# Kernel optimization log

Measured on AMD Instinct MI355X. Metric: run time of the kernel, lower is better.

Reference implementation:

```python
import jax, jax.numpy as jnp
import numpy as np

BATCH, IN_SIZE, CH, DIM, MODES, LAYERS, PROJ, OUT = 16, 1, 128, 128, 32, 4, 128, 1


def setup_inputs() -> dict:
    key = jax.random.key(0)
    ks = jax.random.split(key, 12)
    scale = 1.0 / (CH * CH)
    inp = {
        "z": jax.random.normal(ks[0], (BATCH, IN_SIZE, DIM, DIM), dtype=jnp.float32),
        # Lifting: pointwise linear input_size -> channels
        "lift_w": jax.random.normal(ks[1], (CH, IN_SIZE), dtype=jnp.float32) / np.sqrt(IN_SIZE),
        "lift_b": jnp.zeros((CH,), dtype=jnp.float32),
        # Spectral conv weights per layer, two mode corners, complex stored as real/imag
        "wr1": scale * jax.random.normal(ks[2], (LAYERS, CH, CH, MODES, MODES), dtype=jnp.float32),
        "wi1": scale * jax.random.normal(ks[3], (LAYERS, CH, CH, MODES, MODES), dtype=jnp.float32),
        "wr2": scale * jax.random.normal(ks[4], (LAYERS, CH, CH, MODES, MODES), dtype=jnp.float32),
        "wi2": scale * jax.random.normal(ks[5], (LAYERS, CH, CH, MODES, MODES), dtype=jnp.float32),
        # Projection: channels -> projection_size -> output_size (pointwise MLP)
        "pw1": jax.random.normal(ks[6], (PROJ, CH), dtype=jnp.float32) / np.sqrt(CH),
        "pb1": jnp.zeros((PROJ,), dtype=jnp.float32),
        "pw2": jax.random.normal(ks[7], (OUT, PROJ), dtype=jnp.float32) / np.sqrt(PROJ),
        "pb2": jnp.zeros((OUT,), dtype=jnp.float32),
    }
    return inp


def _spectral_conv(v, w1, w2, modes, size):
    # v: [b, c, X, Y] real; rfft2 over last two dims (norm='backward')
    vf = jnp.fft.rfft2(v, norm="backward")  # [b, c, X, Y//2+1] complex
    of = jnp.zeros_like(vf)
    # low-frequency corner
    of = of.at[:, :, :modes, :modes].set(
        jnp.einsum("bixy,ioxy->boxy", vf[:, :, :modes, :modes], w1))
    # high (negative) frequency corner along first spatial axis
    of = of.at[:, :, -modes:, :modes].set(
        jnp.einsum("bixy,ioxy->boxy", vf[:, :, -modes:, :modes], w2))
    return jnp.fft.irfft2(of, s=(size, size), norm="backward")


def reference(z, lift_w, lift_b, wr1, wi1, wr2, wi2, pw1, pb1, pw2, pb2):
    n_layers = wr1.shape[0]
    modes = wr1.shape[-1]
    size = z.shape[-1]
    # Lifting: [b, in, x, y] -> [b, ch, x, y]
    v = jnp.einsum("bixy,ci->bcxy", z, lift_w) + lift_b[None, :, None, None]
    out = v
    for l in range(n_layers):
        w1 = wr1[l] + 1j * wi1[l]
        w2 = wr2[l] + 1j * wi2[l]
        out = _spectral_conv(out, w1, w2, modes, size)
    # Projection MLP (pointwise over grid)
    h = jnp.einsum("bcxy,pc->bpxy", out, pw1) + pb1[None, :, None, None]
    h = jax.nn.gelu(h)
    out = jnp.einsum("bpxy,op->boxy", h, pw2) + pb2[None, :, None, None]
    return out
```

## Files before the change

### kernel.cpp

```cpp
#include <hip/hip_runtime.h>
#include <math.h>

#define B 16
#define CH 128
#define DIM 128
#define MODES 32
#define NLAYERS 4
#define PROJ 128
#define U 64
#define KY 32
#define NMODE (U*KY)
#define N2 (DIM*DIM)
#define PG 32
#define PPG (PROJ/PG)

__device__ __forceinline__ void async16(const void* g, void* l) {
  __builtin_amdgcn_global_load_lds((const __attribute__((address_space(1))) unsigned int*)g,
                                   (__attribute__((address_space(3))) unsigned int*)l, 16, 0, 0);
}

__global__ __launch_bounds__(256) void k_zf1(const float* __restrict__ z,
                                             float2* __restrict__ t1) {
  __shared__ float zrow[16][DIM];
  __shared__ float2 tw[DIM];
  int bid = blockIdx.x;
  int b = bid >> 3, xt = bid & 7;
  int x0 = xt * 16;
  int t = threadIdx.x;
  if (t < 128) {
    float ang = (float)(2.0 * M_PI) * (float)t / 128.0f;
    tw[t] = make_float2(cosf(ang), sinf(ang));
  }
  for (int e = t; e < 16 * DIM / 4; e += 256)
    ((float4*)&zrow[0][0])[e] = ((const float4*)&z[b * N2 + x0 * DIM])[e];
  __syncthreads();
  #pragma unroll
  for (int j = 0; j < 2; ++j) {
    int it = t + j * 256;
    int x_l = it >> 5, ky = it & 31;
    float tr = 0.f, ti = 0.f;
    for (int y = 0; y < DIM; ++y) {
      float v = zrow[x_l][y];
      float2 w = tw[(ky * y) & 127];
      tr += v * w.x;
      ti -= v * w.y;
    }
    t1[((size_t)b * DIM + x0 + x_l) * KY + ky] = make_float2(tr, ti);
  }
}

__global__ __launch_bounds__(256) void k_zf2(const float2* __restrict__ t1,
                                             float* __restrict__ zfr, float* __restrict__ zfi) {
  __shared__ float2 t1s[DIM][KY];
  __shared__ float2 tw[DIM];
  int bid = blockIdx.x;
  int b = bid >> 1, uh = bid & 1;
  int t = threadIdx.x;
  if (t < 128) {
    float ang = (float)(2.0 * M_PI) * (float)t / 128.0f;
    tw[t] = make_float2(cosf(ang), sinf(ang));
  }
  for (int e = t; e < DIM * KY / 2; e += 256)
    ((float4*)&t1s[0][0])[e] = ((const float4*)&t1[(size_t)b * DIM * KY])[e];
  __syncthreads();
  #pragma unroll
  for (int j = 0; j < 4; ++j) {
    int m = t + j * 256;
    int u_l = m >> 5, ky = m & 31;
    int u = uh * 32 + u_l;
    int kx = (u < 32) ? u : (u + 64);
    float ar = 0.f, ai = 0.f;
    for (int x = 0; x < DIM; ++x) {
      float2 v = t1s[x][ky];
      float2 w = tw[(kx * x) & 127];
      ar += v.x * w.x + v.y * w.y;
      ai += v.y * w.x - v.x * w.y;
    }
    zfr[b * NMODE + u * KY + ky] = ar;
    zfi[b * NMODE + u * KY + ky] = ai;
  }
}

__global__ __launch_bounds__(256) void k_lift(const float* __restrict__ zfr, const float* __restrict__ zfi,
                                              const float* __restrict__ lw, const float* __restrict__ lb,
                                              float2* __restrict__ vcout) {
  int idx = blockIdx.x * 256 + threadIdx.x;
  if (idx >= B * CH * NMODE) return;
  int m = idx & (NMODE - 1);
  int c = (idx >> 11) & 127;
  int b = idx >> 18;
  float w = lw[c];
  float re = w * zfr[b * NMODE + m];
  float im = w * zfi[b * NMODE + m];
  if (m == 0) re += 16384.f * lb[c];
  vcout[idx] = make_float2(re, im);
}

__global__ __launch_bounds__(256) void k_spec(const float2* __restrict__ vc,
                                              const float* __restrict__ wr1, const float* __restrict__ wi1,
                                              const float* __restrict__ wr2, const float* __restrict__ wi2,
                                              float2* __restrict__ oc) {
  __shared__ float4 ring4[4][1024];
  int bid = blockIdx.x;
  int u = ((bid & 7) << 3) | ((bid >> 3) & 7);
  int ot = bid >> 6;
  int o0 = ot * 16;
  int kxw = u & 31;
  const float* wr = (u >= 32) ? wr2 : wr1;
  const float* wi = (u >= 32) ? wi2 : wi1;
  int t = threadIdx.x;
  int ky = t & 31, bh = (t >> 5) & 1, wv = t >> 6;
  int lane = t & 63;
  float accR[4][8] = {}, accI[4][8] = {};

  #define STAGE(c)                                                                   \
    if ((c) < 64) {                                                                  \
      int bf_ = (c) & 3;                                                             \
      int i0_ = (c) * 2;                                                             \
      char* dst0 = (char*)&ring4[0][0] + (size_t)bf_ * 16384;                        \
      _Pragma("unroll")                                                              \
      for (int n = 0; n < 4; ++n) {                                                  \
        int nu = wv * 4 + n;                                                         \
        if (nu < 8) {                                                                \
          int row = nu * 8 + (lane >> 3);                           \
          int ri = row >> 5, il = (row >> 4) & 1, o_l = row & 15;                    \
          int ky4 = (lane & 7) * 4;                                                  \
          const float* src = (ri ? wi : wr) +                                        \
            (((size_t)(i0_ + il) * CH + o0 + o_l) * MODES + kxw) * MODES + ky4;      \
          async16(src, dst0 + (size_t)nu * 1024 + lane * 16);                        \
        } else {                                                                     \
          int nv = nu - 8;                                                           \
          int row = nv * 4 + (lane >> 4);                               \
          int il = row >> 4, bl = row & 15;                                          \
          int ky2 = (lane & 15) * 2;                                                 \
          const float2* src = vc + ((size_t)bl * CH + i0_ + il) * NMODE +            \
                              u * KY + ky2;                                          \
          async16(src, dst0 + 8192 + (size_t)nv * 1024 + lane * 16);                 \
        }                                                                            \
      }                                                                              \
    }

  #define COMPUTE(bf_)                                                               \
    {                                                                                \
      const float*  Wb = (const float*)((const char*)&ring4[0][0] + (size_t)(bf_) * 16384); \
      const float2* Vb = (const float2*)((const char*)&ring4[0][0] + (size_t)(bf_) * 16384 + 8192); \
      _Pragma("unroll")                                                              \
      for (int il = 0; il < 2; ++il) {                                               \
        float wrv[4], wiv[4];                                                        \
        _Pragma("unroll")                                                            \
        for (int j = 0; j < 4; ++j) {                                                \
          wrv[j] = Wb[(il * 16 + wv * 4 + j) * 32 + ky];                             \
          wiv[j] = Wb[((2 + il) * 16 + wv * 4 + j) * 32 + ky];                       \
        }                                                                            \
        _Pragma("unroll")                                                            \
        for (int bb = 0; bb < 8; ++bb) {                                             \
          float2 v = Vb[(il * 16 + bh * 8 + bb) * 32 + ky];                          \
          _Pragma("unroll")                                                          \
          for (int j = 0; j < 4; ++j) {                                              \
            accR[j][bb] += wrv[j] * v.x - wiv[j] * v.y;                              \
            accI[j][bb] += wrv[j] * v.y + wiv[j] * v.x;                              \
          }                                                                          \
        }                                                                            \
      }                                                                              \
    }

  STAGE(0); STAGE(1); STAGE(2);
  for (int k = 0; k < 64; ++k) {
    __builtin_amdgcn_sched_barrier(0);
    if (k < 62)       asm volatile("s_waitcnt vmcnt(8)" ::: "memory");
    else if (k == 62) asm volatile("s_waitcnt vmcnt(4)" ::: "memory");
    else              asm volatile("s_waitcnt vmcnt(0)" ::: "memory");
    __builtin_amdgcn_s_barrier();
    __builtin_amdgcn_sched_barrier(0);
    STAGE(k + 3);
    COMPUTE(k & 3);
  }
  #undef STAGE
  #undef COMPUTE
  #pragma unroll
  for (int j = 0; j < 4; ++j)
    #pragma unroll
    for (int bb = 0; bb < 8; ++bb) {
      int o = o0 + wv * 4 + j, b = bh * 8 + bb;
      oc[(((size_t)b * CH + o) * U + u) * KY + ky] = make_float2(accR[j][bb], accI[j][bb]);
    }
}

__global__ __launch_bounds__(256) void k_proj0(float2* __restrict__ vc) {
  int idx = blockIdx.x * 256 + threadIdx.x;
  if (idx >= B * CH * 33) return;
  int pi = idx % 33;
  int bc = idx / 33;
  float2* base = vc + (size_t)bc * NMODE;
  if (pi == 0) {
    base[0].y = 0.f;
  } else if (pi == 32) {
    base[32 * KY].x *= 0.5f;
    base[32 * KY].y *= 0.5f;
  } else {
    int ua = pi, ub = 64 - pi;
    float2 a = base[ua * KY], b2 = base[ub * KY];
    base[ua * KY] = make_float2(0.5f * (a.x + b2.x), 0.5f * (a.y - b2.y));
    base[ub * KY] = make_float2(0.5f * (b2.x + a.x), 0.5f * (b2.y - a.y));
  }
}

__global__ __launch_bounds__(256) void k_pw1(const float2* __restrict__ xc,
                                             const float* __restrict__ pw1,
                                             float2* __restrict__ hc) {
  __shared__ float wT[CH][CH + 1];
  int bid = blockIdx.x;
  int b = ((bid & 7) << 1) | ((bid >> 8) & 1);
  int jt = (bid >> 3) & 31;
  int t = threadIdx.x;
  for (int e = t; e < CH * CH; e += 256) {
    int p = e >> 7, c = e & 127;
    wT[c][p] = pw1[e];
  }
  __syncthreads();
  int tx = t & 15, ty = t >> 4;
  int j0 = jt * 64 + tx * 4;
  float accR[4][8] = {}, accI[4][8] = {};
  for (int c = 0; c < CH; ++c) {
    const float4* x4 = (const float4*)&xc[((size_t)b * CH + c) * NMODE + j0];
    float4 v0 = x4[0], v1 = x4[1];
    float xrv[4] = {v0.x, v0.z, v1.x, v1.z};
    float xiv[4] = {v0.y, v0.w, v1.y, v1.w};
    float w[8];
    #pragma unroll
    for (int pp = 0; pp < 8; ++pp) w[pp] = wT[c][ty * 8 + pp];
    #pragma unroll
    for (int jj = 0; jj < 4; ++jj)
      #pragma unroll
      for (int pp = 0; pp < 8; ++pp) {
        accR[jj][pp] += w[pp] * xrv[jj];
        accI[jj][pp] += w[pp] * xiv[jj];
      }
  }
  #pragma unroll
  for (int pp = 0; pp < 8; ++pp) {
    int p = ty * 8 + pp;
    float4* o4 = (float4*)&hc[((size_t)b * CH + p) * NMODE + j0];
    o4[0] = make_float4(accR[0][pp], accI[0][pp], accR[1][pp], accI[1][pp]);
    o4[1] = make_float4(accR[2][pp], accI[2][pp], accR[3][pp], accI[3][pp]);
  }
}

__global__ __launch_bounds__(256) void k_idft_partial(const float2* __restrict__ hc,
                                                      const float* __restrict__ pb1,
                                                      const float* __restrict__ pw2,
                                                      float* __restrict__ partial) {
  __shared__ float2 tw[DIM];
  __shared__ float2 hfs[2][NMODE];
  __shared__ float2 sbuf[16][KY];
  __shared__ float4 sE[8][32];
  int bid = blockIdx.x;
  int b = (bid & 7) | (((bid >> 3) & 1) << 3);
  int pg = (bid >> 4) & 31, xs = bid >> 9;
  int x0 = xs * 8;
  int t = threadIdx.x;
  int wv = t >> 6, lane = t & 63;
  if (t < 128) {
    float ang = (float)(2.0 * M_PI) * (float)t / 128.0f;
    tw[t] = make_float2(cosf(ang), sinf(ang));
  }

  #define STAGE_H(bf, pp_)                                                           \
    {                                                                                \
      const char* srcb = (const char*)(hc + ((size_t)b * CH + pg * PPG + (pp_)) * NMODE); \
      _Pragma("unroll")                                                              \
      for (int n = 0; n < 4; ++n) {                                                  \
        int nu = wv * 4 + n;                                                         \
        async16(srcb + (size_t)nu * 1024 + lane * 16,                                \
                (char*)&hfs[bf][0] + (size_t)nu * 1024 + lane * 16);                 \
      }                                                                              \
    }

  STAGE_H(0, 0);
  __syncthreads();
  {
    int xq = t >> 5, j = t & 31;
    int x = x0 + xq;
    int kxE = (j < 16) ? (2 * j) : (2 * j + 64);
    float2 wE = tw[(kxE * x) & 127];
    float2 wO = tw[((kxE + 1) * x) & 127];
    sE[xq][j] = make_float4(wE.x, wE.y, wO.x, wO.y);
  }
  int y = t & 63, xh = t >> 6;
  float Cr[KY], Sr[KY];
  #pragma unroll
  for (int ky = 0; ky < KY; ++ky) {
    float2 w = tw[(ky * y) & 127];
    float wk = (ky == 0) ? 1.f : 2.f;
    Cr[ky] = wk * w.x;
    Sr[ky] = -wk * w.y;
  }
  __syncthreads();
  int xqA = t >> 5, kyA = t & 31;
  float res[8] = {0.f, 0.f, 0.f, 0.f, 0.f, 0.f, 0.f, 0.f};
  for (int pp = 0; pp < PPG; ++pp) {
    int p = pg * PPG + pp;
    int cur = pp & 1;
    if (pp) __syncthreads();
    if (pp + 1 < PPG) STAGE_H(cur ^ 1, pp + 1);
    {
      float per = 0.f, pei = 0.f, por = 0.f, poi = 0.f;
      #pragma unroll
      for (int j = 0; j < 32; ++j) {
        float4 E = sE[xqA][j];
        float2 h0 = hfs[cur][(2 * j) * KY + kyA];
        float2 h1 = hfs[cur][(2 * j + 1) * KY + kyA];
        per += h0.x * E.x - h0.y * E.y;
        pei += h0.x * E.y + h0.y * E.x;
        por += h1.x * E.z - h1.y * E.w;
        poi += h1.x * E.w + h1.y * E.z;
      }
      sbuf[xqA][kyA]     = make_float2(per + por, pei + poi);
      sbuf[xqA + 8][kyA] = make_float2(per - por, pei - poi);
    }
    __syncthreads();
    float pb = pb1[p], pw = pw2[p];
    #pragma unroll
    for (int sl = 0; sl < 4; ++sl) {
      int s_i = xh + sl * 4;
      float ae = 0.f, ao = 0.f;
      #pragma unroll
      for (int ky = 0; ky < KY; ky += 2) {
        float4 v = *(const float4*)&sbuf[s_i][ky];
        ae += v.x * Cr[ky] + v.y * Sr[ky];
        ao += v.z * Cr[ky + 1] + v.w * Sr[ky + 1];
      }
      float hlo = (ae + ao) * (1.f / 16384.f) + pb;
      float hhi = (ae - ao) * (1.f / 16384.f) + pb;
      float zlo = 1.5957691216057308f * (hlo + 0.044715f * hlo * hlo * hlo);
      float zhi = 1.5957691216057308f * (hhi + 0.044715f * hhi * hhi * hhi);
      res[sl * 2]     += pw * hlo * __builtin_amdgcn_rcpf(1.f + __expf(-zlo));
      res[sl * 2 + 1] += pw * hhi * __builtin_amdgcn_rcpf(1.f + __expf(-zhi));
    }
  }
  #undef STAGE_H
  size_t pbase = ((size_t)pg * B + b) * N2;
  #pragma unroll
  for (int sl = 0; sl < 4; ++sl) {
    int s_i = xh + sl * 4;
    int x = x0 + (s_i & 7) + ((s_i >> 3) << 6);
    partial[pbase + x * DIM + y]      = res[sl * 2];
    partial[pbase + x * DIM + y + 64] = res[sl * 2 + 1];
  }
}

__global__ __launch_bounds__(256) void k_reduce(const float* __restrict__ partial,
                                                const float* __restrict__ pb2,
                                                float* __restrict__ outp) {
  int idx = blockIdx.x * 256 + threadIdx.x;
  if (idx >= B * N2) return;
  float s = pb2[0];
  #pragma unroll
  for (int pg = 0; pg < PG; ++pg) s += partial[(size_t)pg * B * N2 + idx];
  outp[idx] = s;
}

extern "C" void kernel_launch(void* const* d_in, const int* in_sizes, int n_in,
                              void* d_out, int out_size, void* d_ws, size_t ws_size,
                              hipStream_t stream) {
  const float* z   = (const float*)d_in[0];
  const float* lw  = (const float*)d_in[1];
  const float* lb  = (const float*)d_in[2];
  const float* wr1 = (const float*)d_in[3];
  const float* wi1 = (const float*)d_in[4];
  const float* wr2 = (const float*)d_in[5];
  const float* wi2 = (const float*)d_in[6];
  const float* pw1 = (const float*)d_in[7];
  const float* pb1 = (const float*)d_in[8];
  const float* pw2 = (const float*)d_in[9];
  const float* pb2 = (const float*)d_in[10];
  float* out = (float*)d_out;
  float* ws = (float*)d_ws;

  float* zfr = ws;
  float* zfi = zfr + 32768;
  float2* Ac = (float2*)(ws + 65536);
  float2* Bc = Ac + (size_t)B * CH * NMODE;
  float2* t1 = Bc;

  k_zf1<<<B * 8, 256, 0, stream>>>(z, t1);
  k_zf2<<<B * 2, 256, 0, stream>>>(t1, zfr, zfi);
  k_lift<<<(B * CH * NMODE) / 256, 256, 0, stream>>>(zfr, zfi, lw, lb, Ac);

  const size_t WSTRIDE = (size_t)CH * CH * MODES * MODES;
  float2 *ir = Ac, *oc = Bc;
  for (int l = 0; l < NLAYERS; ++l) {
    k_spec<<<512, 256, 0, stream>>>(ir,
                                    wr1 + l * WSTRIDE, wi1 + l * WSTRIDE,
                                    wr2 + l * WSTRIDE, wi2 + l * WSTRIDE,
                                    oc);
    if (l < NLAYERS - 1)
      k_proj0<<<(B * CH * 33 + 255) / 256, 256, 0, stream>>>(oc);
    float2* tmp = ir; ir = oc; oc = tmp;
  }
  k_pw1<<<512, 256, 0, stream>>>(ir, pw1, oc);
  float* partial = (float*)ir;
  k_idft_partial<<<B * PG * 8, 256, 0, stream>>>(oc, pb1, pw2, partial);
  k_reduce<<<(B * N2) / 256, 256, 0, stream>>>(partial, pb2, out);
}
```

Baseline: 791.8 us.

## Shrink spectral-mix tiles to 8x8 and launch more blocks with double buffering

The spectral channel-mixing kernel now has each block compute 8 output channels by 8 batches instead of 16 by 16, so four times as many blocks are launched. The explicit 4-deep async ring with hand-placed vmcnt waits is replaced by a simple double buffer synchronised with __syncthreads. The aim is more blocks per CU to hide latency. The cost is that each weight slice is now loaded by two blocks (one per batch half) instead of once, per-block prefetch depth is shallower, and register-level reuse per loaded value is lower.

```diff
diff --git a/kernel.cpp b/kernel.cpp
--- a/kernel.cpp
+++ b/kernel.cpp
@@ -100,61 +100,57 @@
                                               const float* __restrict__ wr1, const float* __restrict__ wi1,
                                               const float* __restrict__ wr2, const float* __restrict__ wi2,
                                               float2* __restrict__ oc) {
-  __shared__ float4 ring4[4][1024];
+  __shared__ float  lW[2][4][8][32];
+  __shared__ float2 lV[2][2][8][32];
   int bid = blockIdx.x;
   int u = ((bid & 7) << 3) | ((bid >> 3) & 7);
-  int ot = bid >> 6;
-  int o0 = ot * 16;
+  int rest = bid >> 6;
+  int o0 = (rest & 15) * 8;
+  int b0 = (rest >> 4) * 8;
   int kxw = u & 31;
   const float* wr = (u >= 32) ? wr2 : wr1;
   const float* wi = (u >= 32) ? wi2 : wi1;
   int t = threadIdx.x;
-  int ky = t & 31, bh = (t >> 5) & 1, wv = t >> 6;
-  int lane = t & 63;
-  float accR[4][8] = {}, accI[4][8] = {};
-
-  #define STAGE(c)                                                                   \
-    if ((c) < 64) {                                                                  \
-      int bf_ = (c) & 3;                                                             \
-      int i0_ = (c) * 2;                                                             \
-      char* dst0 = (char*)&ring4[0][0] + (size_t)bf_ * 16384;                        \
+  int ky = t & 31, q = t >> 5;
+  int oh = q >> 2, bq = q & 3;
+  int wv = t >> 6, lane = t & 63;
+  float accR[4][2] = {}, accI[4][2] = {};
+
+  #define STAGE(bf, i0)                                                              \
+    {                                                                                \
       _Pragma("unroll")                                                              \
-      for (int n = 0; n < 4; ++n) {                                                  \
-        int nu = wv * 4 + n;                                                         \
-        if (nu < 8) {                                                                \
-          int row = nu * 8 + (lane >> 3);                           \
-          int ri = row >> 5, il = (row >> 4) & 1, o_l = row & 15;                    \
-          int ky4 = (lane & 7) * 4;                                                  \
+      for (int n = 0; n < 2; ++n) {                                                  \
+        int nu = wv * 2 + n;                                                         \
+        if (nu < 4) {                                                                \
+          int ri = nu >> 1, il = nu & 1;                                             \
+          int o_l = lane >> 3, ky4 = (lane & 7) * 4;                                 \
           const float* src = (ri ? wi : wr) +                                        \
-            (((size_t)(i0_ + il) * CH + o0 + o_l) * MODES + kxw) * MODES + ky4;      \
-          async16(src, dst0 + (size_t)nu * 1024 + lane * 16);                        \
+            (((size_t)((i0) + il) * CH + o0 + o_l) * MODES + kxw) * MODES + ky4;     \
+          async16(src, (char*)&lW[bf][0][0][0] + (size_t)nu * 1024 + lane * 16);     \
         } else {                                                                     \
-          int nv = nu - 8;                                                           \
-          int row = nv * 4 + (lane >> 4);                               \
-          int il = row >> 4, bl = row & 15;                                          \
-          int ky2 = (lane & 15) * 2;                                                 \
-          const float2* src = vc + ((size_t)bl * CH + i0_ + il) * NMODE +            \
+          int nv = nu - 4;                                                           \
+          int il = nv >> 1, h = nv & 1;                                              \
+          int b_l = h * 4 + (lane >> 4), ky2 = (lane & 15) * 2;                      \
+          const float2* src = vc + ((size_t)(b0 + b_l) * CH + (i0) + il) * NMODE +   \
                               u * KY + ky2;                                          \
-          async16(src, dst0 + 8192 + (size_t)nv * 1024 + lane * 16);                 \
+          async16(src, (char*)&lV[bf][0][0][0] + (size_t)nv * 1024 + lane * 16);     \
         }                                                                            \
       }                                                                              \
     }
 
-  #define COMPUTE(bf_)                                                               \
+  #define COMPUTE(bf)                                                                \
     {                                                                                \
-      const float*  Wb = (const float*)((const char*)&ring4[0][0] + (size_t)(bf_) * 16384); \
-      const float2* Vb = (const float2*)((const char*)&ring4[0][0] + (size_t)(bf_) * 16384 + 8192); \
       _Pragma("unroll")                                                              \
       for (int il = 0; il < 2; ++il) {                                               \
         float wrv[4], wiv[4];                                                        \
         _Pragma("unroll")                                                            \
         for (int j = 0; j < 4; ++j) {                                                \
-          wrv[j] = Wb[(il * 16 + wv * 4 + j) * 32 + ky];                             \
-          wiv[j] = Wb[((2 + il) * 16 + wv * 4 + j) * 32 + ky];                       \
+          wrv[j] = lW[bf][il][oh * 4 + j][ky];                                       \
+          wiv[j] = lW[bf][2 + il][oh * 4 + j][ky];                                   \
         }                                                                            \
         _Pragma("unroll")                                                            \
-        for (int bb = 0; bb < 8; ++bb) {                                             \
-          float2 v = Vb[(il * 16 + bh * 8 + bb) * 32 + ky];                          \
+        for (int bb = 0; bb < 2; ++bb) {                                             \
+          float2 v = lV[bf][il][bq * 2 + bb][ky];                                    \
           _Pragma("unroll")                                                          \
           for (int j = 0; j < 4; ++j) {                                              \
             accR[j][bb] += wrv[j] * v.x - wiv[j] * v.y;                              \
@@ -164,24 +160,20 @@
       }                                                                              \
     }
 
-  STAGE(0); STAGE(1); STAGE(2);
+  STAGE(0, 0);
   for (int k = 0; k < 64; ++k) {
-    __builtin_amdgcn_sched_barrier(0);
-    if (k < 62)       asm volatile("s_waitcnt vmcnt(8)" ::: "memory");
-    else if (k == 62) asm volatile("s_waitcnt vmcnt(4)" ::: "memory");
-    else              asm volatile("s_waitcnt vmcnt(0)" ::: "memory");
-    __builtin_amdgcn_s_barrier();
-    __builtin_amdgcn_sched_barrier(0);
-    STAGE(k + 3);
-    COMPUTE(k & 3);
+    int cur = k & 1;
+    __syncthreads();
+    if (k + 1 < 64) STAGE(cur ^ 1, (k + 1) * 2);
+    COMPUTE(cur);
   }
   #undef STAGE
   #undef COMPUTE
   #pragma unroll
   for (int j = 0; j < 4; ++j)
     #pragma unroll
-    for (int bb = 0; bb < 8; ++bb) {
-      int o = o0 + wv * 4 + j, b = bh * 8 + bb;
+    for (int bb = 0; bb < 2; ++bb) {
+      int o = o0 + oh * 4 + j, b = b0 + bq * 2 + bb;
       oc[(((size_t)b * CH + o) * U + u) * KY + ky] = make_float2(accR[j][bb], accI[j][bb]);
     }
 }
@@ -390,10 +382,10 @@
   const size_t WSTRIDE = (size_t)CH * CH * MODES * MODES;
   float2 *ir = Ac, *oc = Bc;
   for (int l = 0; l < NLAYERS; ++l) {
-    k_spec<<<512, 256, 0, stream>>>(ir,
-                                    wr1 + l * WSTRIDE, wi1 + l * WSTRIDE,
-                                    wr2 + l * WSTRIDE, wi2 + l * WSTRIDE,
-                                    oc);
+    k_spec<<<2048, 256, 0, stream>>>(ir,
+                                     wr1 + l * WSTRIDE, wi1 + l * WSTRIDE,
+                                     wr2 + l * WSTRIDE, wi2 + l * WSTRIDE,
+                                     oc);
     if (l < NLAYERS - 1)
       k_proj0<<<(B * CH * 33 + 255) / 256, 256, 0, stream>>>(oc);
     float2* tmp = ir; ir = oc; oc = tmp;
```

Result: slower. 918.5 us (+16.0%).
